# Kernel tuning notes

Measured on AMD Instinct MI355X. Metric: run time of the kernel, lower is better.

## Reference

```python
import jax, jax.numpy as jnp
import numpy as np

# column-index constants for the node feature matrix and edge attributes
VM, VA, PG, QG, PD, QD = 0, 1, 2, 3, 4, 5
G_COL, B_COL = 0, 1

N_NODES = 100000
N_EDGES = 3200000
N_FEAT = 6


def setup_inputs() -> dict:
    key = jax.random.key(0)
    k1, k2, k3, k4, k5, k6 = jax.random.split(key, 6)
    pred = jax.random.normal(k1, (N_NODES, N_FEAT), dtype=jnp.float32)
    target = jax.random.normal(k2, (N_NODES, N_FEAT), dtype=jnp.float32)
    src = jax.random.randint(k3, (N_EDGES,), 0, N_NODES, dtype=jnp.int32)
    dst = jax.random.randint(k4, (N_EDGES,), 0, N_NODES, dtype=jnp.int32)
    edge_index = jnp.stack([src, dst], axis=0)
    edge_attr = jax.random.normal(k5, (N_EDGES, 2), dtype=jnp.float32)
    mask = jax.random.bernoulli(k6, 0.5, (N_NODES, N_FEAT))
    return {"pred": pred, "target": target, "edge_index": edge_index,
            "edge_attr": edge_attr, "mask": mask}


def reference(pred, target, edge_index, edge_attr, mask):
    # temp_pred[~mask] = target[~mask]
    tp = jnp.where(mask, pred, target)

    V_m = tp[:, VM]
    V_a = tp[:, VA]
    V = V_m * jnp.exp(1j * V_a)           # complex64 [N]
    V_conj = jnp.conj(V)

    # conj(Y_bus) entries on edges: G - jB
    Y_conj = edge_attr[:, G_COL] - 1j * edge_attr[:, B_COL]  # complex64 [E]

    row, col = edge_index[0], edge_index[1]
    # (Y_bus_conj @ V_conj)[i] = sum over edges (i,j) of conj(Y_ij) * conj(V_j)
    msg = Y_conj * V_conj[col]                               # gather-multiply [E]
    matvec = jax.ops.segment_sum(msg, row, num_segments=tp.shape[0])  # scatter-add [N]

    S_injection = V * matvec                                  # diag(V) @ (...)

    net_P = tp[:, PG] - tp[:, PD]
    net_Q = tp[:, QG] - tp[:, QD]
    diff = (net_P + 1j * net_Q) - S_injection

    loss = jnp.mean(jnp.abs(diff))
    real_loss = jnp.mean(jnp.abs(jnp.real(diff)))
    imag_loss = jnp.mean(jnp.abs(jnp.imag(diff)))
    return (loss, real_loss, imag_loss)
```

## Files before the change

kernel.cpp:

```cpp
#include <hip/hip_runtime.h>
#include <hip/hip_fp16.h>
#include <math.h>

constexpr int N_NODES = 100000;
constexpr int N_EDGES = 3200000;
constexpr int NF      = 6;

constexpr int BSHIFT  = 10;
constexpr int BNODES  = 1 << BSHIFT;
constexpr int NB      = (N_NODES + BNODES - 1) >> BSHIFT;
constexpr int CAP     = 33792;
constexpr int NSLICE  = 16;
constexpr int TILE    = 2048;
constexpr int EPT     = TILE / 256;
constexpr int NBLK_PART = (N_EDGES + TILE - 1) / TILE;
constexpr int VPREP_BLOCKS = (N_NODES + 255) / 256;

constexpr size_t MV_BYTES = (size_t)NB * BNODES * 8;
constexpr size_t OFF_V    = 0;
constexpr size_t OFF_REC  = OFF_V  + (size_t)N_NODES * 8;
constexpr size_t OFF_MV   = OFF_REC + (size_t)NB * CAP * 8;
constexpr size_t OFF_CNT  = OFF_MV + MV_BYTES;
constexpr size_t WS_NEED  = OFF_CNT + 1024;

union F2U { float2 f; unsigned long long u; };

__device__ __forceinline__ float2 half2u_to_f2(unsigned u) {
    __half2 h;
    *reinterpret_cast<unsigned*>(&h) = u;
    return __half22float2(h);
}

__global__ __launch_bounds__(256) void partition_edges(
        const int* __restrict__ row, const int* __restrict__ col,
        const float2* __restrict__ attr,
        const float* __restrict__ pred, const float* __restrict__ target,
        const unsigned char* __restrict__ mask,
        float2* __restrict__ v_out,
        unsigned int* __restrict__ gcur,
        uint2* __restrict__ rec_g) {
    __shared__ unsigned int h[4][NB];
    __shared__ unsigned int cur[4][NB];
    __shared__ int wb[4][NB];
    __shared__ int dbase[NB];
    __shared__ unsigned int tot_s[NB];
    __shared__ uint2 rec_s[TILE];
    __shared__ unsigned char bkt_s[TILE];
    __shared__ int total_s;

    const int tid = threadIdx.x;
    const int w = tid >> 6;
    const int e0 = blockIdx.x * TILE;
    const int e_base = e0 + tid * EPT;
    const bool ok = e_base < N_EDGES;

    if (blockIdx.x < VPREP_BLOCKS) {
        int i = blockIdx.x * 256 + tid;
        if (i < N_NODES) {
            const int bb = i * NF;
            float vm = mask[bb + 0] ? pred[bb + 0] : target[bb + 0];
            float va = mask[bb + 1] ? pred[bb + 1] : target[bb + 1];
            float sn, cs;
            sincosf(va, &sn, &cs);
            v_out[i] = make_float2(vm * cs, vm * sn);
        }
    }

    for (int i = tid; i < 4 * NB; i += 256) {
        (&h[0][0])[i] = 0u;
        (&cur[0][0])[i] = 0u;
    }
    __syncthreads();

    int r[EPT];
    if (ok) {
        int4 ra = *(const int4*)(row + e_base);
        int4 rb = *(const int4*)(row + e_base + 4);
        r[0]=ra.x; r[1]=ra.y; r[2]=ra.z; r[3]=ra.w;
        r[4]=rb.x; r[5]=rb.y; r[6]=rb.z; r[7]=rb.w;
        #pragma unroll
        for (int k = 0; k < EPT; ++k)
            atomicAdd(&h[w][r[k] >> BSHIFT], 1u);
    }
    __syncthreads();

    if (tid < NB)
        tot_s[tid] = h[0][tid] + h[1][tid] + h[2][tid] + h[3][tid];
    __syncthreads();

    if (tid < NB) {
        int lbase = 0;
        for (int j = 0; j < tid; ++j) lbase += (int)tot_s[j];
        unsigned t0 = h[0][tid], t1 = h[1][tid], t2 = h[2][tid];
        unsigned tot = tot_s[tid];
        unsigned g = tot ? atomicAdd(&gcur[tid], tot) : 0u;
        dbase[tid] = (int)g - lbase;
        wb[0][tid] = lbase;
        wb[1][tid] = lbase + (int)t0;
        wb[2][tid] = lbase + (int)(t0 + t1);
        wb[3][tid] = lbase + (int)(t0 + t1 + t2);
        if (tid == NB - 1) total_s = lbase + (int)tot;
    }
    __syncthreads();

    if (ok) {
        int4 ca = *(const int4*)(col + e_base);
        int4 cb = *(const int4*)(col + e_base + 4);
        int c[EPT] = {ca.x, ca.y, ca.z, ca.w, cb.x, cb.y, cb.z, cb.w};
        float4 a0 = *(const float4*)(attr + e_base);
        float4 a1 = *(const float4*)(attr + e_base + 2);
        float4 a2 = *(const float4*)(attr + e_base + 4);
        float4 a3 = *(const float4*)(attr + e_base + 6);
        float gx[EPT] = {a0.x, a0.z, a1.x, a1.z, a2.x, a2.z, a3.x, a3.z};
        float gy[EPT] = {a0.y, a0.w, a1.y, a1.w, a2.y, a2.w, a3.y, a3.w};
        #pragma unroll
        for (int k = 0; k < EPT; ++k) {
            int rr = r[k];
            int b = rr >> BSHIFT;
            int slot = wb[w][b] + (int)atomicAdd(&cur[w][b], 1u);
            __half2 hh = __floats2half2_rn(gx[k], gy[k]);
            rec_s[slot] = make_uint2(
                (unsigned)c[k] | ((unsigned)(rr & (BNODES - 1)) << 17),
                *reinterpret_cast<unsigned int*>(&hh));
            bkt_s[slot] = (unsigned char)b;
        }
    }
    __syncthreads();

    const int total = total_s;
    for (int j = tid; j < total; j += 256) {
        int b = (int)bkt_s[j];
        int g = dbase[b] + j;
        if (g < CAP)
            rec_g[(size_t)b * CAP + g] = rec_s[j];
    }
}

__global__ __launch_bounds__(256) void accum_finalize(
        const unsigned int* __restrict__ gcur,
        const uint2* __restrict__ rec,
        float* __restrict__ mv,
        unsigned int* __restrict__ sdone,
        float* __restrict__ sums,
        unsigned int* __restrict__ done_all,
        const float* __restrict__ pred,
        const float* __restrict__ target,
        const unsigned char* __restrict__ mask,
        const float2* __restrict__ v,
        float* __restrict__ out) {
    __shared__ float acc_re[BNODES];
    __shared__ float acc_im[BNODES];
    __shared__ unsigned int old_s;
    const int tid = threadIdx.x;
    const int b = blockIdx.x / NSLICE;
    const int s = blockIdx.x % NSLICE;
    int cnt = (int)min(gcur[b], (unsigned)CAP);
    for (int i = tid; i < BNODES; i += 256) { acc_re[i] = 0.f; acc_im[i] = 0.f; }
    __syncthreads();
    int per = (((cnt + NSLICE - 1) / NSLICE) + 3) & ~3;
    int st = s * per;
    int en = min(st + per, cnt);
    const uint2* rp = rec + (size_t)b * CAP;
    int j = st + 4 * tid;
    for (; j + 3 < en; j += 1024) {
        uint4 q0 = *(const uint4*)(rp + j);
        uint4 q1 = *(const uint4*)(rp + j + 2);
        int c0 = (int)(q0.x & 0x1FFFFu), li0 = (int)(q0.x >> 17);
        int c1 = (int)(q0.z & 0x1FFFFu), li1 = (int)(q0.z >> 17);
        int c2 = (int)(q1.x & 0x1FFFFu), li2 = (int)(q1.x >> 17);
        int c3 = (int)(q1.z & 0x1FFFFu), li3 = (int)(q1.z >> 17);
        float2 vv0 = v[c0];
        float2 vv1 = v[c1];
        float2 vv2 = v[c2];
        float2 vv3 = v[c3];
        float2 gb0 = half2u_to_f2(q0.y);
        float2 gb1 = half2u_to_f2(q0.w);
        float2 gb2 = half2u_to_f2(q1.y);
        float2 gb3 = half2u_to_f2(q1.w);
        atomicAdd(&acc_re[li0], fmaf(gb0.x, vv0.x, -gb0.y * vv0.y));
        atomicAdd(&acc_im[li0], -fmaf(gb0.x, vv0.y, gb0.y * vv0.x));
        atomicAdd(&acc_re[li1], fmaf(gb1.x, vv1.x, -gb1.y * vv1.y));
        atomicAdd(&acc_im[li1], -fmaf(gb1.x, vv1.y, gb1.y * vv1.x));
        atomicAdd(&acc_re[li2], fmaf(gb2.x, vv2.x, -gb2.y * vv2.y));
        atomicAdd(&acc_im[li2], -fmaf(gb2.x, vv2.y, gb2.y * vv2.x));
        atomicAdd(&acc_re[li3], fmaf(gb3.x, vv3.x, -gb3.y * vv3.y));
        atomicAdd(&acc_im[li3], -fmaf(gb3.x, vv3.y, gb3.y * vv3.x));
    }
    for (; j < en; ++j) {
        uint2 q = rp[j];
        int c0 = (int)(q.x & 0x1FFFFu), li0 = (int)(q.x >> 17);
        float2 vv0 = v[c0];
        float2 gb0 = half2u_to_f2(q.y);
        atomicAdd(&acc_re[li0], fmaf(gb0.x, vv0.x, -gb0.y * vv0.y));
        atomicAdd(&acc_im[li0], -fmaf(gb0.x, vv0.y, gb0.y * vv0.x));
    }
    __syncthreads();
    {
        float* mvb = mv + (((size_t)b << BSHIFT) << 1);
        for (int i = tid; i < BNODES; i += 256) {
            float r = acc_re[i];
            float q = acc_im[i];
            if (r != 0.f || q != 0.f) {
                atomicAdd(&mvb[2 * i],     r);
                atomicAdd(&mvb[2 * i + 1], q);
            }
        }
    }
    asm volatile("s_waitcnt vmcnt(0)" ::: "memory");
    __syncthreads();
    if (tid == 0)
        old_s = __hip_atomic_fetch_add(&sdone[b], 1u, __ATOMIC_RELAXED,
                                       __HIP_MEMORY_SCOPE_AGENT);
    __syncthreads();
    if (old_s != (unsigned)(NSLICE - 1)) return;

    const unsigned long long* pb =
        reinterpret_cast<const unsigned long long*>(mv) + ((size_t)b << BSHIFT);
    float a = 0.f, ar = 0.f, ai = 0.f;
    for (int li = tid; li < BNODES; li += 256) {
        int i = (b << BSHIFT) + li;
        if (i >= N_NODES) break;
        F2U cvt;
        cvt.u = __hip_atomic_load(&pb[li], __ATOMIC_RELAXED,
                                  __HIP_MEMORY_SCOPE_AGENT);
        float mr = cvt.f.x, mi = cvt.f.y;
        const int bb = i * NF;
        float pg = mask[bb + 2] ? pred[bb + 2] : target[bb + 2];
        float qg = mask[bb + 3] ? pred[bb + 3] : target[bb + 3];
        float pd = mask[bb + 4] ? pred[bb + 4] : target[bb + 4];
        float qd = mask[bb + 5] ? pred[bb + 5] : target[bb + 5];
        float netP = pg - pd;
        float netQ = qg - qd;
        float2 vv = v[i];
        float s_re = vv.x * mr - vv.y * mi;
        float s_im = vv.x * mi + vv.y * mr;
        float dre = netP - s_re;
        float dim = netQ - s_im;
        ar += fabsf(dre);
        ai += fabsf(dim);
        a  += sqrtf(dre * dre + dim * dim);
    }
    #pragma unroll
    for (int off = 32; off > 0; off >>= 1) {
        a  += __shfl_down(a,  off, 64);
        ar += __shfl_down(ar, off, 64);
        ai += __shfl_down(ai, off, 64);
    }
    __shared__ float red[3][4];
    int wave = tid >> 6;
    int lane = tid & 63;
    if (lane == 0) { red[0][wave] = a; red[1][wave] = ar; red[2][wave] = ai; }
    __syncthreads();
    if (tid == 0) {
        float r0 = atomicAdd(&sums[0], red[0][0] + red[0][1] + red[0][2] + red[0][3]);
        float r1 = atomicAdd(&sums[1], red[1][0] + red[1][1] + red[1][2] + red[1][3]);
        float r2 = atomicAdd(&sums[2], red[2][0] + red[2][1] + red[2][2] + red[2][3]);
        float chk = r0 + r1 + r2;
        if (chk == chk) {
            unsigned fin = atomicAdd(done_all, 1u);
            if (fin == (unsigned)(NB - 1)) {
                const float inv = 1.0f / (float)N_NODES;
                float t0 = atomicAdd(&sums[0], 0.f);
                float t1 = atomicAdd(&sums[1], 0.f);
                float t2 = atomicAdd(&sums[2], 0.f);
                __hip_atomic_store(&out[0], t0 * inv, __ATOMIC_RELAXED, __HIP_MEMORY_SCOPE_AGENT);
                __hip_atomic_store(&out[1], t1 * inv, __ATOMIC_RELAXED, __HIP_MEMORY_SCOPE_AGENT);
                __hip_atomic_store(&out[2], t2 * inv, __ATOMIC_RELAXED, __HIP_MEMORY_SCOPE_AGENT);
            }
        }
    }
}

__global__ void node_prep_fb(const float* __restrict__ pred,
                             const float* __restrict__ target,
                             const unsigned char* __restrict__ mask,
                             float2* __restrict__ v) {
    int i = blockIdx.x * blockDim.x + threadIdx.x;
    if (i >= N_NODES) return;
    const int b = i * NF;
    float vm = mask[b + 0] ? pred[b + 0] : target[b + 0];
    float va = mask[b + 1] ? pred[b + 1] : target[b + 1];
    float s, c;
    sincosf(va, &s, &c);
    v[i] = make_float2(vm * c, vm * s);
}

__global__ void edge_scatter_fb(const int* __restrict__ row,
                                const int* __restrict__ col,
                                const float2* __restrict__ attr,
                                const float2* __restrict__ v,
                                float2* __restrict__ mv) {
    int e = blockIdx.x * blockDim.x + threadIdx.x;
    if (e >= N_EDGES) return;
    int r = row[e];
    int c = col[e];
    float2 gb = attr[e];
    float2 vv = v[c];
    float mre = fmaf(gb.x, vv.x, -gb.y * vv.y);
    float mim = -fmaf(gb.x, vv.y, gb.y * vv.x);
    atomicAdd(&mv[r].x, mre);
    atomicAdd(&mv[r].y, mim);
}

__global__ void finalize_fb(const float* __restrict__ pred,
                            const float* __restrict__ target,
                            const unsigned char* __restrict__ mask,
                            const float2* __restrict__ v,
                            const float2* __restrict__ mv,
                            float* __restrict__ sums) {
    int i = blockIdx.x * blockDim.x + threadIdx.x;
    float a = 0.f, ar = 0.f, ai = 0.f;
    if (i < N_NODES) {
        const int b = i * NF;
        float pg = mask[b + 2] ? pred[b + 2] : target[b + 2];
        float qg = mask[b + 3] ? pred[b + 3] : target[b + 3];
        float pd = mask[b + 4] ? pred[b + 4] : target[b + 4];
        float qd = mask[b + 5] ? pred[b + 5] : target[b + 5];
        float netP = pg - pd;
        float netQ = qg - qd;
        float2 vv = v[i];
        float2 m = mv[i];
        float s_re = vv.x * m.x - vv.y * m.y;
        float s_im = vv.x * m.y + vv.y * m.x;
        float dre = netP - s_re;
        float dim = netQ - s_im;
        ar = fabsf(dre);
        ai = fabsf(dim);
        a  = sqrtf(dre * dre + dim * dim);
    }
    #pragma unroll
    for (int off = 32; off > 0; off >>= 1) {
        a  += __shfl_down(a,  off, 64);
        ar += __shfl_down(ar, off, 64);
        ai += __shfl_down(ai, off, 64);
    }
    __shared__ float red[3][4];
    int wave = threadIdx.x >> 6;
    int lane = threadIdx.x & 63;
    if (lane == 0) { red[0][wave] = a; red[1][wave] = ar; red[2][wave] = ai; }
    __syncthreads();
    if (threadIdx.x == 0) {
        atomicAdd(&sums[0], red[0][0] + red[0][1] + red[0][2] + red[0][3]);
        atomicAdd(&sums[1], red[1][0] + red[1][1] + red[1][2] + red[1][3]);
        atomicAdd(&sums[2], red[2][0] + red[2][1] + red[2][2] + red[2][3]);
    }
}

__global__ void write_out_fb(const float* __restrict__ sums, float* __restrict__ out) {
    if (threadIdx.x == 0 && blockIdx.x == 0) {
        const float inv = 1.0f / (float)N_NODES;
        out[0] = sums[0] * inv;
        out[1] = sums[1] * inv;
        out[2] = sums[2] * inv;
    }
}

extern "C" void kernel_launch(void* const* d_in, const int* in_sizes, int n_in,
                              void* d_out, int out_size, void* d_ws, size_t ws_size,
                              hipStream_t stream) {
    const float*         pred   = (const float*)d_in[0];
    const float*         target = (const float*)d_in[1];
    const int*           eidx   = (const int*)d_in[2];
    const float2*        attr   = (const float2*)d_in[3];
    const unsigned char* mask   = (const unsigned char*)d_in[4];
    float* out = (float*)d_out;

    const int* row = eidx;
    const int* col = eidx + N_EDGES;

    char* ws = (char*)d_ws;
    const int B = 256;

    if (ws_size >= WS_NEED) {
        float2*             v        = (float2*)(ws + OFF_V);
        uint2*              rec_g    = (uint2*)(ws + OFF_REC);
        float*              mv       = (float*)(ws + OFF_MV);
        unsigned int*       gcur     = (unsigned int*)(ws + OFF_CNT);
        unsigned int*       sdone    = (unsigned int*)(ws + OFF_CNT + 512);
        float*              sums     = (float*)(ws + OFF_CNT + 912);
        unsigned int*       done_all = (unsigned int*)(ws + OFF_CNT + 928);

        hipMemsetAsync(ws + OFF_MV, 0, MV_BYTES + 1024, stream);
        partition_edges<<<NBLK_PART, B, 0, stream>>>(row, col, attr,
                                                     pred, target, mask, v,
                                                     gcur, rec_g);
        accum_finalize<<<NB * NSLICE, B, 0, stream>>>(gcur, rec_g, mv,
                                                      sdone, sums, done_all,
                                                      pred, target, mask, v, out);
    } else {
        float2* v    = (float2*)ws;
        float2* mv   = (float2*)(ws + (size_t)N_NODES * 8);
        float*  sums = (float*)(ws + 2ull * N_NODES * 8);
        hipMemsetAsync(mv, 0, (size_t)N_NODES * 8 + 16, stream);
        node_prep_fb<<<(N_NODES + B - 1) / B, B, 0, stream>>>(pred, target, mask, v);
        edge_scatter_fb<<<(N_EDGES + B - 1) / B, B, 0, stream>>>(row, col, attr, v, mv);
        finalize_fb<<<(N_NODES + B - 1) / B, B, 0, stream>>>(pred, target, mask, v, mv, sums);
        write_out_fb<<<1, 64, 0, stream>>>(sums, out);
    }
}
```

Baseline: 185.3 us.

## Compute edge messages during partitioning and store full-precision products

The gather of V[col] and the complex multiply move from the accumulate kernel into the partition kernel, which now writes finished fp32 messages plus a separate 16-bit local-index array instead of packed col/half-precision admittance records. V preparation moves to its own kernel, which also zeroes the matvec buffer, so the memset shrinks to the counters. Slices per bucket drop from 16 to 8. The accumulate pass then does only streaming loads and LDS atomics, at the cost of 10 bytes per edge instead of 8, an extra launch, and random gathers moved into partitioning. Keeping the products in fp32 also removes the earlier fp16 rounding of G and B.

Measured after the change: 195.7 us. 5.6% more time.

```diff
diff --git a/kernel.cpp b/kernel.cpp
--- a/kernel.cpp
+++ b/kernel.cpp
@@ -10,7 +10,7 @@
 constexpr int BNODES  = 1 << BSHIFT;
 constexpr int NB      = (N_NODES + BNODES - 1) >> BSHIFT;
 constexpr int CAP     = 33792;
-constexpr int NSLICE  = 16;
+constexpr int NSLICE  = 8;
 constexpr int TILE    = 2048;
 constexpr int EPT     = TILE / 256;
 constexpr int NBLK_PART = (N_EDGES + TILE - 1) / TILE;
@@ -18,33 +18,46 @@
 
 constexpr size_t MV_BYTES = (size_t)NB * BNODES * 8;
 constexpr size_t OFF_V    = 0;
-constexpr size_t OFF_REC  = OFF_V  + (size_t)N_NODES * 8;
-constexpr size_t OFF_MV   = OFF_REC + (size_t)NB * CAP * 8;
+constexpr size_t OFF_A    = OFF_V + (size_t)N_NODES * 8;
+constexpr size_t OFF_L    = OFF_A + (size_t)NB * CAP * 8;
+constexpr size_t OFF_MV   = OFF_L + (size_t)NB * CAP * 2;
 constexpr size_t OFF_CNT  = OFF_MV + MV_BYTES;
 constexpr size_t WS_NEED  = OFF_CNT + 1024;
 
 union F2U { float2 f; unsigned long long u; };
 
-__device__ __forceinline__ float2 half2u_to_f2(unsigned u) {
-    __half2 h;
-    *reinterpret_cast<unsigned*>(&h) = u;
-    return __half22float2(h);
+__global__ __launch_bounds__(256) void node_prep(
+        const float* __restrict__ pred,
+        const float* __restrict__ target,
+        const unsigned char* __restrict__ mask,
+        float2* __restrict__ v,
+        float* __restrict__ mv) {
+    int i = blockIdx.x * blockDim.x + threadIdx.x;
+    for (int k = i; k < NB * BNODES * 2; k += VPREP_BLOCKS * 256)
+        mv[k] = 0.f;
+    if (i >= N_NODES) return;
+    const int b = i * NF;
+    float vm = mask[b + 0] ? pred[b + 0] : target[b + 0];
+    float va = mask[b + 1] ? pred[b + 1] : target[b + 1];
+    float s, c;
+    sincosf(va, &s, &c);
+    v[i] = make_float2(vm * c, vm * s);
 }
 
 __global__ __launch_bounds__(256) void partition_edges(
         const int* __restrict__ row, const int* __restrict__ col,
         const float2* __restrict__ attr,
-        const float* __restrict__ pred, const float* __restrict__ target,
-        const unsigned char* __restrict__ mask,
-        float2* __restrict__ v_out,
+        const float2* __restrict__ v,
         unsigned int* __restrict__ gcur,
-        uint2* __restrict__ rec_g) {
+        float2* __restrict__ Ag,
+        unsigned short* __restrict__ Lg) {
     __shared__ unsigned int h[4][NB];
     __shared__ unsigned int cur[4][NB];
     __shared__ int wb[4][NB];
     __shared__ int dbase[NB];
     __shared__ unsigned int tot_s[NB];
-    __shared__ uint2 rec_s[TILE];
+    __shared__ float2 rec_s[TILE];
+    __shared__ unsigned short li_s[TILE];
     __shared__ unsigned char bkt_s[TILE];
     __shared__ int total_s;
 
@@ -53,18 +66,6 @@
     const int e0 = blockIdx.x * TILE;
     const int e_base = e0 + tid * EPT;
     const bool ok = e_base < N_EDGES;
-
-    if (blockIdx.x < VPREP_BLOCKS) {
-        int i = blockIdx.x * 256 + tid;
-        if (i < N_NODES) {
-            const int bb = i * NF;
-            float vm = mask[bb + 0] ? pred[bb + 0] : target[bb + 0];
-            float va = mask[bb + 1] ? pred[bb + 1] : target[bb + 1];
-            float sn, cs;
-            sincosf(va, &sn, &cs);
-            v_out[i] = make_float2(vm * cs, vm * sn);
-        }
-    }
 
     for (int i = tid; i < 4 * NB; i += 256) {
         (&h[0][0])[i] = 0u;
@@ -107,6 +108,9 @@
         int4 ca = *(const int4*)(col + e_base);
         int4 cb = *(const int4*)(col + e_base + 4);
         int c[EPT] = {ca.x, ca.y, ca.z, ca.w, cb.x, cb.y, cb.z, cb.w};
+        float2 vv[EPT];
+        #pragma unroll
+        for (int k = 0; k < EPT; ++k) vv[k] = v[c[k]];
         float4 a0 = *(const float4*)(attr + e_base);
         float4 a1 = *(const float4*)(attr + e_base + 2);
         float4 a2 = *(const float4*)(attr + e_base + 4);
@@ -118,10 +122,10 @@
             int rr = r[k];
             int b = rr >> BSHIFT;
             int slot = wb[w][b] + (int)atomicAdd(&cur[w][b], 1u);
-            __half2 hh = __floats2half2_rn(gx[k], gy[k]);
-            rec_s[slot] = make_uint2(
-                (unsigned)c[k] | ((unsigned)(rr & (BNODES - 1)) << 17),
-                *reinterpret_cast<unsigned int*>(&hh));
+            float mre = fmaf(gx[k], vv[k].x, -gy[k] * vv[k].y);
+            float mim = -fmaf(gx[k], vv[k].y, gy[k] * vv[k].x);
+            rec_s[slot] = make_float2(mre, mim);
+            li_s[slot]  = (unsigned short)(rr & (BNODES - 1));
             bkt_s[slot] = (unsigned char)b;
         }
     }
@@ -131,14 +135,18 @@
     for (int j = tid; j < total; j += 256) {
         int b = (int)bkt_s[j];
         int g = dbase[b] + j;
-        if (g < CAP)
-            rec_g[(size_t)b * CAP + g] = rec_s[j];
+        if (g < CAP) {
+            size_t o = (size_t)b * CAP + g;
+            Ag[o] = rec_s[j];
+            Lg[o] = li_s[j];
+        }
     }
 }
 
 __global__ __launch_bounds__(256) void accum_finalize(
         const unsigned int* __restrict__ gcur,
-        const uint2* __restrict__ rec,
+        const float2* __restrict__ Ag,
+        const unsigned short* __restrict__ Lg,
         float* __restrict__ mv,
         unsigned int* __restrict__ sdone,
         float* __restrict__ sums,
@@ -160,39 +168,27 @@
     int per = (((cnt + NSLICE - 1) / NSLICE) + 3) & ~3;
     int st = s * per;
     int en = min(st + per, cnt);
-    const uint2* rp = rec + (size_t)b * CAP;
+    const float2* ap = Ag + (size_t)b * CAP;
+    const unsigned short* lp = Lg + (size_t)b * CAP;
     int j = st + 4 * tid;
     for (; j + 3 < en; j += 1024) {
-        uint4 q0 = *(const uint4*)(rp + j);
-        uint4 q1 = *(const uint4*)(rp + j + 2);
-        int c0 = (int)(q0.x & 0x1FFFFu), li0 = (int)(q0.x >> 17);
-        int c1 = (int)(q0.z & 0x1FFFFu), li1 = (int)(q0.z >> 17);
-        int c2 = (int)(q1.x & 0x1FFFFu), li2 = (int)(q1.x >> 17);
-        int c3 = (int)(q1.z & 0x1FFFFu), li3 = (int)(q1.z >> 17);
-        float2 vv0 = v[c0];
-        float2 vv1 = v[c1];
-        float2 vv2 = v[c2];
-        float2 vv3 = v[c3];
-        float2 gb0 = half2u_to_f2(q0.y);
-        float2 gb1 = half2u_to_f2(q0.w);
-        float2 gb2 = half2u_to_f2(q1.y);
-        float2 gb3 = half2u_to_f2(q1.w);
-        atomicAdd(&acc_re[li0], fmaf(gb0.x, vv0.x, -gb0.y * vv0.y));
-        atomicAdd(&acc_im[li0], -fmaf(gb0.x, vv0.y, gb0.y * vv0.x));
-        atomicAdd(&acc_re[li1], fmaf(gb1.x, vv1.x, -gb1.y * vv1.y));
-        atomicAdd(&acc_im[li1], -fmaf(gb1.x, vv1.y, gb1.y * vv1.x));
-        atomicAdd(&acc_re[li2], fmaf(gb2.x, vv2.x, -gb2.y * vv2.y));
-        atomicAdd(&acc_im[li2], -fmaf(gb2.x, vv2.y, gb2.y * vv2.x));
-        atomicAdd(&acc_re[li3], fmaf(gb3.x, vv3.x, -gb3.y * vv3.y));
-        atomicAdd(&acc_im[li3], -fmaf(gb3.x, vv3.y, gb3.y * vv3.x));
+        float4 m01 = *(const float4*)(ap + j);
+        float4 m23 = *(const float4*)(ap + j + 2);
+        ushort4 l4 = *(const ushort4*)(lp + j);
+        atomicAdd(&acc_re[l4.x], m01.x);
+        atomicAdd(&acc_im[l4.x], m01.y);
+        atomicAdd(&acc_re[l4.y], m01.z);
+        atomicAdd(&acc_im[l4.y], m01.w);
+        atomicAdd(&acc_re[l4.z], m23.x);
+        atomicAdd(&acc_im[l4.z], m23.y);
+        atomicAdd(&acc_re[l4.w], m23.z);
+        atomicAdd(&acc_im[l4.w], m23.w);
     }
     for (; j < en; ++j) {
-        uint2 q = rp[j];
-        int c0 = (int)(q.x & 0x1FFFFu), li0 = (int)(q.x >> 17);
-        float2 vv0 = v[c0];
-        float2 gb0 = half2u_to_f2(q.y);
-        atomicAdd(&acc_re[li0], fmaf(gb0.x, vv0.x, -gb0.y * vv0.y));
-        atomicAdd(&acc_im[li0], -fmaf(gb0.x, vv0.y, gb0.y * vv0.x));
+        float2 m = ap[j];
+        int li = (int)lp[j];
+        atomicAdd(&acc_re[li], m.x);
+        atomicAdd(&acc_im[li], m.y);
     }
     __syncthreads();
     {
@@ -373,18 +369,19 @@
 
     if (ws_size >= WS_NEED) {
         float2*             v        = (float2*)(ws + OFF_V);
-        uint2*              rec_g    = (uint2*)(ws + OFF_REC);
+        float2*             Ag       = (float2*)(ws + OFF_A);
+        unsigned short*     Lg       = (unsigned short*)(ws + OFF_L);
         float*              mv       = (float*)(ws + OFF_MV);
         unsigned int*       gcur     = (unsigned int*)(ws + OFF_CNT);
         unsigned int*       sdone    = (unsigned int*)(ws + OFF_CNT + 512);
         float*              sums     = (float*)(ws + OFF_CNT + 912);
         unsigned int*       done_all = (unsigned int*)(ws + OFF_CNT + 928);
 
-        hipMemsetAsync(ws + OFF_MV, 0, MV_BYTES + 1024, stream);
-        partition_edges<<<NBLK_PART, B, 0, stream>>>(row, col, attr,
-                                                     pred, target, mask, v,
-                                                     gcur, rec_g);
-        accum_finalize<<<NB * NSLICE, B, 0, stream>>>(gcur, rec_g, mv,
+        hipMemsetAsync(ws + OFF_CNT, 0, 1024, stream);
+        node_prep<<<VPREP_BLOCKS, B, 0, stream>>>(pred, target, mask, v, mv);
+        partition_edges<<<NBLK_PART, B, 0, stream>>>(row, col, attr, v,
+                                                     gcur, Ag, Lg);
+        accum_finalize<<<NB * NSLICE, B, 0, stream>>>(gcur, Ag, Lg, mv,
                                                       sdone, sums, done_all,
                                                       pred, target, mask, v, out);
     } else {
```
